# Kernel tuning notes

Measured on AMD Instinct MI355X. Metric: run time of the kernel, lower is better.

Reference implementation:

```python
import jax, jax.numpy as jnp
import numpy as np

N_NODES = 40000
N_EDGES = 640000
F_IN = 128
HID = 128
N_CLASSES = 10
N_GRAPHS = 64


def _gcn_conv(x, row, col, norm, W, b, n_nodes):
    h = x @ W                                   # [N, H]
    msg = h[row] * norm[:, None]                # [E+N, H] gather + scale
    out = jax.ops.segment_sum(msg, col, num_segments=n_nodes)  # scatter-add
    return out + b


def setup_inputs() -> dict:
    key = jax.random.key(0)
    ks = jax.random.split(key, 8)
    x = jax.random.normal(ks[0], (N_NODES, F_IN), dtype=jnp.float32)
    edge_index = jax.random.randint(ks[1], (2, N_EDGES), 0, N_NODES, dtype=jnp.int32)
    batch = jnp.sort(jax.random.randint(ks[2], (N_NODES,), 0, N_GRAPHS, dtype=jnp.int32))
    s1 = 1.0 / np.sqrt(F_IN)
    s2 = 1.0 / np.sqrt(HID)
    W1 = jax.random.normal(ks[3], (F_IN, HID), dtype=jnp.float32) * s1
    W2 = jax.random.normal(ks[4], (HID, HID), dtype=jnp.float32) * s2
    W3 = jax.random.normal(ks[5], (HID, HID), dtype=jnp.float32) * s2
    Wl = jax.random.normal(ks[6], (HID, N_CLASSES), dtype=jnp.float32) * s2
    b1 = jnp.zeros((HID,), jnp.float32)
    b2 = jnp.zeros((HID,), jnp.float32)
    b3 = jnp.zeros((HID,), jnp.float32)
    bl = jnp.zeros((N_CLASSES,), jnp.float32)
    return {"x": x, "edge_index": edge_index, "batch": batch,
            "W1": W1, "b1": b1, "W2": W2, "b2": b2, "W3": W3, "b3": b3,
            "Wl": Wl, "bl": bl}


def reference(x, edge_index, batch, W1, b1, W2, b2, W3, b3, Wl, bl):
    n = x.shape[0]
    # add self-loops (PyG add_remaining_self_loops with weight 1)
    loops = jnp.arange(n, dtype=edge_index.dtype)
    row = jnp.concatenate([edge_index[0], loops])
    col = jnp.concatenate([edge_index[1], loops])
    w = jnp.ones(row.shape, dtype=x.dtype)
    # symmetric normalization: deg over target nodes incl. self-loops
    deg = jax.ops.segment_sum(w, col, num_segments=n)
    dis = jnp.where(deg > 0, jax.lax.rsqrt(deg), 0.0)
    norm = dis[row] * dis[col]                  # [E+N]

    h = jax.nn.relu(_gcn_conv(x, row, col, norm, W1, b1, n))
    h = jax.nn.relu(_gcn_conv(h, row, col, norm, W2, b2, n))
    h = jax.nn.relu(_gcn_conv(h, row, col, norm, W3, b3, n))

    # global mean pool over graph ids
    sums = jax.ops.segment_sum(h, batch, num_segments=N_GRAPHS)      # [G, H]
    cnts = jax.ops.segment_sum(jnp.ones((n,), h.dtype), batch, num_segments=N_GRAPHS)
    pooled = sums / jnp.maximum(cnts, 1.0)[:, None]
    # dropout(p=0.2) is identity in eval mode
    return pooled @ Wl + bl                     # [G, num_classes]
```

## Files before the change

kernel.cpp:

```cpp
#include <hip/hip_runtime.h>
#include <hip/hip_bf16.h>

#define N_NODES   40000
#define N_EDGES   640000
#define F         128
#define N_GRAPHS  64
#define N_CLASSES 10

typedef short bf16x8 __attribute__((ext_vector_type(8)));
typedef float f32x4  __attribute__((ext_vector_type(4)));

__device__ __forceinline__ unsigned short f2bf(float f) {
    union { float f; unsigned u; } v; v.f = f;
    unsigned r = v.u + 0x7fffu + ((v.u >> 16) & 1u);
    return (unsigned short)(r >> 16);
}
__device__ __forceinline__ float bflo(unsigned u) { return __uint_as_float(u << 16); }
__device__ __forceinline__ float bfhi(unsigned u) { return __uint_as_float(u & 0xffff0000u); }
__device__ __forceinline__ unsigned pack2(float a, float b) {
    return (unsigned)f2bf(a) | ((unsigned)f2bf(b) << 16);
}

#define APITCH 136

#define PANEL_U4  ((size_t)N_NODES * 8)

__global__ void wcvt_kernel(const float* __restrict__ W1, const float* __restrict__ W2,
                            const float* __restrict__ W3, unsigned short* __restrict__ Wt,
                            int* __restrict__ deg, int* __restrict__ tks) {
    int idx = blockIdx.x * 256 + threadIdx.x;
    if (idx < N_NODES) deg[idx] = 0;
    if (idx < 2) tks[idx] = 0;
    int l = idx >> 14;
    int r = idx & 16383;
    int c = r >> 7, k = r & 127;
    const float* W = (l == 0) ? W1 : ((l == 1) ? W2 : W3);
    Wt[idx] = f2bf(W[k * 128 + c]);
}

#define SCAN_BLOCKS 40
#define SCAN_CHUNK  1000
__global__ __launch_bounds__(256) void scan_kernel(
    const int* __restrict__ deg, int* __restrict__ rowptr,
    int* __restrict__ cursor, float* __restrict__ dis,
    float* __restrict__ pooled_zero, int* __restrict__ chunkSum,
    int* __restrict__ ticket) {
    __shared__ int wpart[4];
    __shared__ int blockBase;
    const int tid  = threadIdx.x;
    const int lane = tid & 63;
    const int wave = tid >> 6;
    const int b    = blockIdx.x;
    const int base = b * SCAN_CHUNK;

    for (int k = b * 256 + tid; k < N_GRAPHS * F + N_GRAPHS; k += SCAN_BLOCKS * 256)
        pooled_zero[k] = 0.f;

    int4 d = make_int4(0, 0, 0, 0);
    if (tid < 250) d = *(const int4*)(deg + base + tid * 4);
    const int sown = d.x + d.y + d.z + d.w;

    int s = sown;
#pragma unroll
    for (int off = 1; off < 64; off <<= 1) {
        int n = __shfl_up(s, off, 64);
        if (lane >= off) s += n;
    }
    if (lane == 63) wpart[wave] = s;
    __syncthreads();

    if (tid == 0) {
        int run = 0;
#pragma unroll
        for (int w = 0; w < 4; ++w) { int t = wpart[w]; wpart[w] = run; run += t; }
        atomicExch(&chunkSum[b], run);
        __threadfence();
        atomicAdd(ticket, 1);
        while (atomicAdd(ticket, 0) < SCAN_BLOCKS) { }
    }
    __syncthreads();

    if (wave == 0) {
        int cs = (lane < SCAN_BLOCKS) ? atomicAdd(&chunkSum[lane], 0) : 0;
        int sc_ = cs;
#pragma unroll
        for (int off = 1; off < 64; off <<= 1) {
            int n = __shfl_up(sc_, off, 64);
            if (lane >= off) sc_ += n;
        }
        int bb = __shfl(sc_, (b == 0) ? 0 : b - 1, 64);
        if (lane == 0) blockBase = (b == 0) ? 0 : bb;
    }
    __syncthreads();

    if (tid < 250) {
        int excl = blockBase + wpart[wave] + (s - sown);
        int4 r;
        r.x = excl;
        r.y = r.x + d.x;
        r.z = r.y + d.y;
        r.w = r.z + d.z;
        *(int4*)(rowptr + base + tid * 4) = r;
        *(int4*)(cursor + base + tid * 4) = r;
        float4 di;
        di.x = rsqrtf((float)d.x + 1.0f);
        di.y = rsqrtf((float)d.y + 1.0f);
        di.z = rsqrtf((float)d.z + 1.0f);
        di.w = rsqrtf((float)d.w + 1.0f);
        *(float4*)(dis + base + tid * 4) = di;
    }
}

__global__ void fill_kernel(const int* __restrict__ row, const int* __restrict__ col,
                            int* __restrict__ cursor, int* __restrict__ csr_src) {
    int e = blockIdx.x * 256 + threadIdx.x;
    if (e < N_EDGES) {
        int pos = atomicAdd(&cursor[col[e]], 1);
        csr_src[pos] = row[e];
    }
}

template<bool ABF16, bool RELU, bool SCALE, bool COUNT>
__global__ __launch_bounds__(256) void gemm_mfma(
    const void* __restrict__ Araw, const unsigned short* __restrict__ Wt,
    const float* __restrict__ bias, const float* __restrict__ dis,
    unsigned short* __restrict__ Hb,
    const int* __restrict__ cnt_col, int* __restrict__ cnt_deg) {
    __shared__ unsigned short As[64 * APITCH];
    __shared__ unsigned short Ws[64 * APITCH];
    const int tid  = threadIdx.x;
    const int row0 = blockIdx.x * 64;

    if (COUNT) {
        int t = (blockIdx.x * 256 + tid) * 4;
#pragma unroll
        for (int j = 0; j < 4; ++j) atomicAdd(&cnt_deg[cnt_col[t + j]], 1);
    }

    {
        const uint4* src = (const uint4*)Wt;
#pragma unroll
        for (int j = 0; j < 4; ++j) {
            int c4 = tid + j * 256;
            int c  = c4 >> 4;
            int o  = c4 & 15;
            *(uint4*)(Ws + c * APITCH + o * 8) = src[c4];
        }
    }
    if (ABF16) {
        const uint4* src = (const uint4*)Araw;
#pragma unroll
        for (int j = 0; j < 4; ++j) {
            int c4 = tid + j * 256;
            int r  = c4 >> 4;
            int p  = c4 & 15;
            int o  = p << 3;
            uint4 hv = src[(size_t)(p >> 3) * PANEL_U4 + (size_t)(row0 + r) * 8 + (p & 7)];
            float f0 = bflo(hv.x), f1 = bfhi(hv.x), f2 = bflo(hv.y), f3 = bfhi(hv.y);
            float f4_ = bflo(hv.z), f5 = bfhi(hv.z), f6 = bflo(hv.w), f7 = bfhi(hv.w);
            if (bias) {
                float4 b0 = *(const float4*)(bias + o);
                float4 b1 = *(const float4*)(bias + o + 4);
                f0 += b0.x; f1 += b0.y; f2 += b0.z; f3 += b0.w;
                f4_ += b1.x; f5 += b1.y; f6 += b1.z; f7 += b1.w;
            }
            if (RELU) {
                f0 = fmaxf(f0, 0.f); f1 = fmaxf(f1, 0.f); f2 = fmaxf(f2, 0.f);
                f3 = fmaxf(f3, 0.f); f4_ = fmaxf(f4_, 0.f); f5 = fmaxf(f5, 0.f);
                f6 = fmaxf(f6, 0.f); f7 = fmaxf(f7, 0.f);
            }
            uint4 pk;
            pk.x = pack2(f0, f1); pk.y = pack2(f2, f3);
            pk.z = pack2(f4_, f5); pk.w = pack2(f6, f7);
            *(uint4*)(As + r * APITCH + o) = pk;
        }
    } else {
        const float* A = (const float*)Araw;
#pragma unroll
        for (int j = 0; j < 8; ++j) {
            int c4 = tid + j * 256;
            int r  = c4 >> 5;
            int o  = (c4 & 31) << 2;
            float4 v = *(const float4*)(A + (size_t)(row0 + r) * F + o);
            if (bias) {
                v.x += bias[o + 0]; v.y += bias[o + 1];
                v.z += bias[o + 2]; v.w += bias[o + 3];
            }
            if (RELU) {
                v.x = fmaxf(v.x, 0.f); v.y = fmaxf(v.y, 0.f);
                v.z = fmaxf(v.z, 0.f); v.w = fmaxf(v.w, 0.f);
            }
            uint2 p;
            p.x = pack2(v.x, v.y);
            p.y = pack2(v.z, v.w);
            *(uint2*)(As + r * APITCH + o) = p;
        }
    }
    __syncthreads();

    const int lane = tid & 63;
    const int wave = tid >> 6;
    const int m16  = lane & 15;
    const int quad = lane >> 4;

    f32x4 acc[8];
#pragma unroll
    for (int t = 0; t < 8; ++t) acc[t] = (f32x4)(0.0f);

    bf16x8 afrag[4];
#pragma unroll
    for (int kk = 0; kk < 4; ++kk)
        afrag[kk] = *(const bf16x8*)(As + (wave * 16 + m16) * APITCH + kk * 32 + quad * 8);

#pragma unroll
    for (int kk = 0; kk < 4; ++kk) {
#pragma unroll
        for (int t = 0; t < 4; ++t) {
            bf16x8 b = *(const bf16x8*)(Ws + (t * 16 + m16) * APITCH + kk * 32 + quad * 8);
            acc[t] = __builtin_amdgcn_mfma_f32_16x16x32_bf16(afrag[kk], b, acc[t], 0, 0, 0);
        }
    }
    __syncthreads();

    {
        const uint4* src = (const uint4*)Wt + 1024;
#pragma unroll
        for (int j = 0; j < 4; ++j) {
            int c4 = tid + j * 256;
            int c  = c4 >> 4;
            int o  = c4 & 15;
            *(uint4*)(Ws + c * APITCH + o * 8) = src[c4];
        }
    }
    __syncthreads();

#pragma unroll
    for (int kk = 0; kk < 4; ++kk) {
#pragma unroll
        for (int t = 0; t < 4; ++t) {
            bf16x8 b = *(const bf16x8*)(Ws + (t * 16 + m16) * APITCH + kk * 32 + quad * 8);
            acc[4 + t] = __builtin_amdgcn_mfma_f32_16x16x32_bf16(afrag[kk], b, acc[4 + t], 0, 0, 0);
        }
    }

    const int rloc = wave * 16 + quad * 4;
    float sc[4];
#pragma unroll
    for (int rg = 0; rg < 4; ++rg) sc[rg] = SCALE ? dis[row0 + rloc + rg] : 1.0f;
#pragma unroll
    for (int t = 0; t < 8; ++t) {
        int col = t * 16 + m16;
#pragma unroll
        for (int rg = 0; rg < 4; ++rg)
            As[(rloc + rg) * APITCH + col] = f2bf(acc[t][rg] * sc[rg]);
    }
#pragma unroll
    for (int i = 0; i < 4; ++i) {
        int idx = lane + i * 64;
        int r   = idx >> 4;
        int p   = idx & 15;
        uint4 val = *(const uint4*)(As + (wave * 16 + r) * APITCH + p * 8);
        *((uint4*)Hb + (size_t)(p >> 3) * PANEL_U4
                     + (size_t)(row0 + wave * 16 + r) * 8 + (p & 7)) = val;
    }
}

template <bool SCALED>
__global__ __launch_bounds__(256) void gather_kernel(
    const unsigned short* __restrict__ Hb, const int* __restrict__ csr_src,
    const int* __restrict__ rowptr, const int* __restrict__ deg,
    const float* __restrict__ dis, unsigned short* __restrict__ AGGb,
    int pass) {
    const int grp  = threadIdx.x >> 3;
    const int v    = blockIdx.x * 32 + grp;
    const int c8   = threadIdx.x & 7;

    const int start = rowptr[v];
    const int len   = deg[v];
    const uint4* Hp   = (const uint4*)Hb + (size_t)pass * PANEL_U4 + c8;
    uint4*       AGGp = (uint4*)AGGb + (size_t)pass * PANEL_U4 + c8;

    float acc[8];
#pragma unroll
    for (int i = 0; i < 8; ++i) acc[i] = 0.f;

    const int jmain = len & ~3;
    int j = 0;
    for (; j < jmain; j += 4) {
        int   r[4];
        uint4 h[4];
        float w[4];
#pragma unroll
        for (int u = 0; u < 4; ++u) r[u] = csr_src[start + j + u];
#pragma unroll
        for (int u = 0; u < 4; ++u) h[u] = Hp[(size_t)r[u] * 8];
#pragma unroll
        for (int u = 0; u < 4; ++u) w[u] = SCALED ? dis[r[u]] : 1.0f;
#pragma unroll
        for (int u = 0; u < 4; ++u) {
            acc[0] = fmaf(bflo(h[u].x), w[u], acc[0]);
            acc[1] = fmaf(bfhi(h[u].x), w[u], acc[1]);
            acc[2] = fmaf(bflo(h[u].y), w[u], acc[2]);
            acc[3] = fmaf(bfhi(h[u].y), w[u], acc[3]);
            acc[4] = fmaf(bflo(h[u].z), w[u], acc[4]);
            acc[5] = fmaf(bfhi(h[u].z), w[u], acc[5]);
            acc[6] = fmaf(bflo(h[u].w), w[u], acc[6]);
            acc[7] = fmaf(bfhi(h[u].w), w[u], acc[7]);
        }
    }
    if (j < len) {
        int   r[4];
        uint4 h[4];
        float w[4];
#pragma unroll
        for (int u = 0; u < 4; ++u) {
            int  sl    = j + u;
            bool valid = sl < len;
            r[u] = csr_src[start + (valid ? sl : len - 1)];
            w[u] = valid ? (SCALED ? dis[r[u]] : 1.0f) : 0.0f;
        }
#pragma unroll
        for (int u = 0; u < 4; ++u) h[u] = Hp[(size_t)r[u] * 8];
#pragma unroll
        for (int u = 0; u < 4; ++u) {
            acc[0] = fmaf(bflo(h[u].x), w[u], acc[0]);
            acc[1] = fmaf(bfhi(h[u].x), w[u], acc[1]);
            acc[2] = fmaf(bflo(h[u].y), w[u], acc[2]);
            acc[3] = fmaf(bfhi(h[u].y), w[u], acc[3]);
            acc[4] = fmaf(bflo(h[u].z), w[u], acc[4]);
            acc[5] = fmaf(bfhi(h[u].z), w[u], acc[5]);
            acc[6] = fmaf(bflo(h[u].w), w[u], acc[6]);
            acc[7] = fmaf(bfhi(h[u].w), w[u], acc[7]);
        }
    }

    {
        float dc  = dis[v];
        float ws_ = SCALED ? dc : 1.0f;
        uint4 h = Hp[(size_t)v * 8];
        acc[0] = fmaf(bflo(h.x), ws_, acc[0]); acc[1] = fmaf(bfhi(h.x), ws_, acc[1]);
        acc[2] = fmaf(bflo(h.y), ws_, acc[2]); acc[3] = fmaf(bfhi(h.y), ws_, acc[3]);
        acc[4] = fmaf(bflo(h.z), ws_, acc[4]); acc[5] = fmaf(bfhi(h.z), ws_, acc[5]);
        acc[6] = fmaf(bflo(h.w), ws_, acc[6]); acc[7] = fmaf(bfhi(h.w), ws_, acc[7]);
        uint4 pk;
        pk.x = pack2(acc[0] * dc, acc[1] * dc);
        pk.y = pack2(acc[2] * dc, acc[3] * dc);
        pk.z = pack2(acc[4] * dc, acc[5] * dc);
        pk.w = pack2(acc[6] * dc, acc[7] * dc);
        AGGp[(size_t)v * 8] = pk;
    }
}

#define POOL_NODES 100
__global__ __launch_bounds__(256) void pool_kernel(
    const unsigned short* __restrict__ AGGb, const int* __restrict__ batch,
    const float* __restrict__ b3,
    float* __restrict__ pooled, float* __restrict__ cnt) {
    const int tid  = threadIdx.x;
    const int f4   = (tid & 31) << 2;
    const int slot = tid >> 5;
    const int base = blockIdx.x * POOL_NODES;
    const float4 bf = *(const float4*)(b3 + f4);
    const unsigned short* Ap = AGGb + (size_t)(f4 >> 6) * N_NODES * 64 + (f4 & 63);

    float4 acc = make_float4(0.f, 0.f, 0.f, 0.f);
    float c = 0.f;
    int gcur = -1;
    for (int j = slot; j < POOL_NODES; j += 8) {
        int v = base + j;
        int g = batch[v];
        if (g != gcur) {
            if (gcur >= 0) {
                float* dst = pooled + gcur * F + f4;
                atomicAdd(dst + 0, acc.x); atomicAdd(dst + 1, acc.y);
                atomicAdd(dst + 2, acc.z); atomicAdd(dst + 3, acc.w);
                if (f4 == 0) atomicAdd(&cnt[gcur], c);
            }
            acc = make_float4(0.f, 0.f, 0.f, 0.f); c = 0.f; gcur = g;
        }
        uint2 a = *(const uint2*)(Ap + (size_t)v * 64);
        acc.x += fmaxf(bflo(a.x) + bf.x, 0.f);
        acc.y += fmaxf(bfhi(a.x) + bf.y, 0.f);
        acc.z += fmaxf(bflo(a.y) + bf.z, 0.f);
        acc.w += fmaxf(bfhi(a.y) + bf.w, 0.f);
        c += 1.f;
    }
    if (gcur >= 0) {
        float* dst = pooled + gcur * F + f4;
        atomicAdd(dst + 0, acc.x); atomicAdd(dst + 1, acc.y);
        atomicAdd(dst + 2, acc.z); atomicAdd(dst + 3, acc.w);
        if (f4 == 0) atomicAdd(&cnt[gcur], c);
    }
}

__global__ void head_kernel(const float* __restrict__ pooled,
                            const float* __restrict__ cnt,
                            const float* __restrict__ Wl,
                            const float* __restrict__ bl,
                            float* __restrict__ out) {
    int tid = threadIdx.x;
    if (tid >= N_GRAPHS * N_CLASSES) return;
    int g = tid / N_CLASSES, c = tid % N_CLASSES;
    float acc = 0.f;
    for (int ff = 0; ff < F; ++ff)
        acc += pooled[g * F + ff] * Wl[ff * N_CLASSES + c];
    out[g * N_CLASSES + c] = acc / fmaxf(cnt[g], 1.f) + bl[c];
}

extern "C" void kernel_launch(void* const* d_in, const int* in_sizes, int n_in,
                              void* d_out, int out_size, void* d_ws, size_t ws_size,
                              hipStream_t stream) {
    const float* x    = (const float*)d_in[0];
    const int*   ei   = (const int*)d_in[1];
    const int*   bat  = (const int*)d_in[2];
    const float* W1   = (const float*)d_in[3];
    const float* b1   = (const float*)d_in[4];
    const float* W2   = (const float*)d_in[5];
    const float* b2   = (const float*)d_in[6];
    const float* W3   = (const float*)d_in[7];
    const float* b3   = (const float*)d_in[8];
    const float* Wl   = (const float*)d_in[9];
    const float* bl   = (const float*)d_in[10];
    float* out = (float*)d_out;

    const int* row = ei;
    const int* col = ei + N_EDGES;

    float*          ws      = (float*)d_ws;
    float*          dis     = ws;
    unsigned short* Hb      = (unsigned short*)(dis + N_NODES);
    unsigned short* AGGb    = Hb + (size_t)N_NODES * F;
    float*          pooled  = (float*)(AGGb + (size_t)N_NODES * F);
    float*          cnt     = pooled + N_GRAPHS * F;
    int*            deg     = (int*)(cnt + N_GRAPHS);
    int*            rowptr  = deg + N_NODES;
    int*            cursor  = rowptr + N_NODES;
    int*            csr_src = cursor + N_NODES;
    unsigned short* Wtb     = (unsigned short*)(csr_src + N_EDGES);
    int*            chunkSum= (int*)(Wtb + 3 * 16384);
    int*            tks     = chunkSum + SCAN_BLOCKS;

    const int edgeGrid   = (N_EDGES + 255) / 256;
    const int gemmGrid   = N_NODES / 64;
    const int gatherGrid = N_NODES / 32;

    wcvt_kernel<<<192, 256, 0, stream>>>(W1, W2, W3, Wtb, deg, tks);

    gemm_mfma<false, false, false, true><<<gemmGrid, 256, 0, stream>>>(
        x, Wtb, nullptr, nullptr, Hb, col, deg);
    scan_kernel<<<SCAN_BLOCKS, 256, 0, stream>>>(deg, rowptr, cursor, dis,
                                                 pooled, chunkSum, &tks[0]);
    fill_kernel<<<edgeGrid, 256, 0, stream>>>(row, col, cursor, csr_src);
    gather_kernel<true><<<gatherGrid, 256, 0, stream>>>(Hb, csr_src, rowptr, deg, dis, AGGb, 0);
    gather_kernel<true><<<gatherGrid, 256, 0, stream>>>(Hb, csr_src, rowptr, deg, dis, AGGb, 1);

    gemm_mfma<true, true, true, false><<<gemmGrid, 256, 0, stream>>>(
        AGGb, Wtb + 16384, b1, dis, Hb, nullptr, nullptr);
    gather_kernel<false><<<gatherGrid, 256, 0, stream>>>(Hb, csr_src, rowptr, deg, dis, AGGb, 0);
    gather_kernel<false><<<gatherGrid, 256, 0, stream>>>(Hb, csr_src, rowptr, deg, dis, AGGb, 1);

    gemm_mfma<true, true, true, false><<<gemmGrid, 256, 0, stream>>>(
        AGGb, Wtb + 32768, b2, dis, Hb, nullptr, nullptr);
    gather_kernel<false><<<gatherGrid, 256, 0, stream>>>(Hb, csr_src, rowptr, deg, dis, AGGb, 0);
    gather_kernel<false><<<gatherGrid, 256, 0, stream>>>(Hb, csr_src, rowptr, deg, dis, AGGb, 1);

    pool_kernel<<<N_NODES / POOL_NODES, 256, 0, stream>>>(AGGb, bat, b3, pooled, cnt);
    head_kernel<<<1, N_GRAPHS * N_CLASSES, 0, stream>>>(pooled, cnt, Wl, bl, out);
}
```

Baseline: 291.7 us.

## Split feature panels into four 32-column slices and use nontemporal CSR/output access

The bf16 node-feature layout changes from two 64-column panels to four 32-column panels, and each gather pass now handles one 32-feature slice with 4 threads per node. The aim is to shrink each pass's random-gather working set (40000 x 64 bytes) so it fits better in L2/MALL cache. CSR index loads and aggregated-output stores are also marked nontemporal so they do not pollute the cache. In exchange, every layer reads the CSR structure twice as many times and launches twice as many gather kernels.

```diff
diff --git a/kernel.cpp b/kernel.cpp
--- a/kernel.cpp
+++ b/kernel.cpp
@@ -9,6 +9,7 @@
 
 typedef short bf16x8 __attribute__((ext_vector_type(8)));
 typedef float f32x4  __attribute__((ext_vector_type(4)));
+typedef unsigned int u32x4 __attribute__((ext_vector_type(4)));
 
 __device__ __forceinline__ unsigned short f2bf(float f) {
     union { float f; unsigned u; } v; v.f = f;
@@ -23,7 +24,7 @@
 
 #define APITCH 136
 
-#define PANEL_U4  ((size_t)N_NODES * 8)
+#define PANEL_U4Q ((size_t)N_NODES * 4)
 
 __global__ void wcvt_kernel(const float* __restrict__ W1, const float* __restrict__ W2,
                             const float* __restrict__ W3, unsigned short* __restrict__ Wt,
@@ -155,7 +156,7 @@
             int r  = c4 >> 4;
             int p  = c4 & 15;
             int o  = p << 3;
-            uint4 hv = src[(size_t)(p >> 3) * PANEL_U4 + (size_t)(row0 + r) * 8 + (p & 7)];
+            uint4 hv = src[(size_t)(p >> 2) * PANEL_U4Q + (size_t)(row0 + r) * 4 + (p & 3)];
             float f0 = bflo(hv.x), f1 = bfhi(hv.x), f2 = bflo(hv.y), f3 = bfhi(hv.y);
             float f4_ = bflo(hv.z), f5 = bfhi(hv.z), f6 = bflo(hv.w), f7 = bfhi(hv.w);
             if (bias) {
@@ -260,8 +261,8 @@
         int r   = idx >> 4;
         int p   = idx & 15;
         uint4 val = *(const uint4*)(As + (wave * 16 + r) * APITCH + p * 8);
-        *((uint4*)Hb + (size_t)(p >> 3) * PANEL_U4
-                     + (size_t)(row0 + wave * 16 + r) * 8 + (p & 7)) = val;
+        *((uint4*)Hb + (size_t)(p >> 2) * PANEL_U4Q
+                     + (size_t)(row0 + wave * 16 + r) * 4 + (p & 3)) = val;
     }
 }
 
@@ -271,14 +272,14 @@
     const int* __restrict__ rowptr, const int* __restrict__ deg,
     const float* __restrict__ dis, unsigned short* __restrict__ AGGb,
     int pass) {
-    const int grp  = threadIdx.x >> 3;
-    const int v    = blockIdx.x * 32 + grp;
-    const int c8   = threadIdx.x & 7;
+    const int grp  = threadIdx.x >> 2;
+    const int v    = blockIdx.x * 64 + grp;
+    const int c4   = threadIdx.x & 3;
 
     const int start = rowptr[v];
     const int len   = deg[v];
-    const uint4* Hp   = (const uint4*)Hb + (size_t)pass * PANEL_U4 + c8;
-    uint4*       AGGp = (uint4*)AGGb + (size_t)pass * PANEL_U4 + c8;
+    const uint4* Hp   = (const uint4*)Hb + (size_t)pass * PANEL_U4Q + c4;
+    uint4*       AGGp = (uint4*)AGGb + (size_t)pass * PANEL_U4Q + c4;
 
     float acc[8];
 #pragma unroll
@@ -291,9 +292,10 @@
         uint4 h[4];
         float w[4];
 #pragma unroll
-        for (int u = 0; u < 4; ++u) r[u] = csr_src[start + j + u];
-#pragma unroll
-        for (int u = 0; u < 4; ++u) h[u] = Hp[(size_t)r[u] * 8];
+        for (int u = 0; u < 4; ++u)
+            r[u] = __builtin_nontemporal_load(csr_src + start + j + u);
+#pragma unroll
+        for (int u = 0; u < 4; ++u) h[u] = Hp[(size_t)r[u] * 4];
 #pragma unroll
         for (int u = 0; u < 4; ++u) w[u] = SCALED ? dis[r[u]] : 1.0f;
 #pragma unroll
@@ -316,11 +318,11 @@
         for (int u = 0; u < 4; ++u) {
             int  sl    = j + u;
             bool valid = sl < len;
-            r[u] = csr_src[start + (valid ? sl : len - 1)];
+            r[u] = __builtin_nontemporal_load(csr_src + start + (valid ? sl : len - 1));
             w[u] = valid ? (SCALED ? dis[r[u]] : 1.0f) : 0.0f;
         }
 #pragma unroll
-        for (int u = 0; u < 4; ++u) h[u] = Hp[(size_t)r[u] * 8];
+        for (int u = 0; u < 4; ++u) h[u] = Hp[(size_t)r[u] * 4];
 #pragma unroll
         for (int u = 0; u < 4; ++u) {
             acc[0] = fmaf(bflo(h[u].x), w[u], acc[0]);
@@ -337,17 +339,17 @@
     {
         float dc  = dis[v];
         float ws_ = SCALED ? dc : 1.0f;
-        uint4 h = Hp[(size_t)v * 8];
+        uint4 h = Hp[(size_t)v * 4];
         acc[0] = fmaf(bflo(h.x), ws_, acc[0]); acc[1] = fmaf(bfhi(h.x), ws_, acc[1]);
         acc[2] = fmaf(bflo(h.y), ws_, acc[2]); acc[3] = fmaf(bfhi(h.y), ws_, acc[3]);
         acc[4] = fmaf(bflo(h.z), ws_, acc[4]); acc[5] = fmaf(bfhi(h.z), ws_, acc[5]);
         acc[6] = fmaf(bflo(h.w), ws_, acc[6]); acc[7] = fmaf(bfhi(h.w), ws_, acc[7]);
-        uint4 pk;
+        u32x4 pk;
         pk.x = pack2(acc[0] * dc, acc[1] * dc);
         pk.y = pack2(acc[2] * dc, acc[3] * dc);
         pk.z = pack2(acc[4] * dc, acc[5] * dc);
         pk.w = pack2(acc[6] * dc, acc[7] * dc);
-        AGGp[(size_t)v * 8] = pk;
+        __builtin_nontemporal_store(pk, (u32x4*)(AGGp + (size_t)v * 4));
     }
 }
 
@@ -361,7 +363,7 @@
     const int slot = tid >> 5;
     const int base = blockIdx.x * POOL_NODES;
     const float4 bf = *(const float4*)(b3 + f4);
-    const unsigned short* Ap = AGGb + (size_t)(f4 >> 6) * N_NODES * 64 + (f4 & 63);
+    const unsigned short* Ap = AGGb + (size_t)(f4 >> 5) * N_NODES * 32 + (f4 & 31);
 
     float4 acc = make_float4(0.f, 0.f, 0.f, 0.f);
     float c = 0.f;
@@ -378,7 +380,7 @@
             }
             acc = make_float4(0.f, 0.f, 0.f, 0.f); c = 0.f; gcur = g;
         }
-        uint2 a = *(const uint2*)(Ap + (size_t)v * 64);
+        uint2 a = *(const uint2*)(Ap + (size_t)v * 32);
         acc.x += fmaxf(bflo(a.x) + bf.x, 0.f);
         acc.y += fmaxf(bfhi(a.x) + bf.y, 0.f);
         acc.z += fmaxf(bflo(a.y) + bf.z, 0.f);
@@ -442,7 +444,7 @@
 
     const int edgeGrid   = (N_EDGES + 255) / 256;
     const int gemmGrid   = N_NODES / 64;
-    const int gatherGrid = N_NODES / 32;
+    const int gatherGrid = N_NODES / 64;
 
     wcvt_kernel<<<192, 256, 0, stream>>>(W1, W2, W3, Wtb, deg, tks);
 
@@ -451,18 +453,19 @@
     scan_kernel<<<SCAN_BLOCKS, 256, 0, stream>>>(deg, rowptr, cursor, dis,
                                                  pooled, chunkSum, &tks[0]);
     fill_kernel<<<edgeGrid, 256, 0, stream>>>(row, col, cursor, csr_src);
-    gather_kernel<true><<<gatherGrid, 256, 0, stream>>>(Hb, csr_src, rowptr, deg, dis, AGGb, 0);
-    gather_kernel<true><<<gatherGrid, 256, 0, stream>>>(Hb, csr_src, rowptr, deg, dis, AGGb, 1);
+#pragma unroll
+    for (int p = 0; p < 4; ++p)
+        gather_kernel<true><<<gatherGrid, 256, 0, stream>>>(Hb, csr_src, rowptr, deg, dis, AGGb, p);
 
     gemm_mfma<true, true, true, false><<<gemmGrid, 256, 0, stream>>>(
         AGGb, Wtb + 16384, b1, dis, Hb, nullptr, nullptr);
-    gather_kernel<false><<<gatherGrid, 256, 0, stream>>>(Hb, csr_src, rowptr, deg, dis, AGGb, 0);
-    gather_kernel<false><<<gatherGrid, 256, 0, stream>>>(Hb, csr_src, rowptr, deg, dis, AGGb, 1);
+    for (int p = 0; p < 4; ++p)
+        gather_kernel<false><<<gatherGrid, 256, 0, stream>>>(Hb, csr_src, rowptr, deg, dis, AGGb, p);
 
     gemm_mfma<true, true, true, false><<<gemmGrid, 256, 0, stream>>>(
         AGGb, Wtb + 32768, b2, dis, Hb, nullptr, nullptr);
-    gather_kernel<false><<<gatherGrid, 256, 0, stream>>>(Hb, csr_src, rowptr, deg, dis, AGGb, 0);
-    gather_kernel<false><<<gatherGrid, 256, 0, stream>>>(Hb, csr_src, rowptr, deg, dis, AGGb, 1);
+    for (int p = 0; p < 4; ++p)
+        gather_kernel<false><<<gatherGrid, 256, 0, stream>>>(Hb, csr_src, rowptr, deg, dis, AGGb, p);
 
     pool_kernel<<<N_NODES / POOL_NODES, 256, 0, stream>>>(AGGb, bat, b3, pooled, cnt);
     head_kernel<<<1, N_GRAPHS * N_CLASSES, 0, stream>>>(pooled, cnt, Wl, bl, out);
```

After: 374.0 us. 28.2% more time.
